# Kernel optimization log

Hardware: AMD Instinct MI355X
Metric: run time of the kernel (lower is better)

The kernel has to match this reference:

```python
import jax, jax.numpy as jnp
import numpy as np

H = 256      # hidden_dim
D = 64       # dim_dynamic
ND = 2       # num_dynamic
PR = 7       # pooler_resolution
S = PR * PR  # 49 spatial positions
B = 4800     # N * nr_boxes
P = H * D    # num_params
EPS = 1e-5


def setup_inputs() -> dict:
    key = jax.random.key(0)
    ks = jax.random.split(key, 32)
    def w(k, shape):
        return jax.random.normal(k, shape, dtype=jnp.float32) * 0.02
    inp = {
        "pro_features": jax.random.normal(ks[0], (1, B, H), jnp.float32),
        "roi_features": jax.random.normal(ks[1], (S, B, H), jnp.float32),
        "pos_xywh": jax.random.normal(ks[2], (1, B, H), jnp.float32),
        "pos_img": jax.random.normal(ks[3], (S, B, H), jnp.float32),
        "pos_local": jax.random.uniform(ks[4], (PR, PR), jnp.float32),
        "bboxes_xywh": jax.random.uniform(ks[5], (B, 4), jnp.float32, minval=0.2, maxval=1.0),
        # dynamic_layer: H -> ND*P
        "Wd": w(ks[6], (H, ND * P)), "bd": jnp.zeros((ND * P,), jnp.float32),
        # query_scale MLP (2 layers, H->H->H)
        "Wqs1": w(ks[7], (H, H)), "bqs1": jnp.zeros((H,), jnp.float32),
        "Wqs2": w(ks[8], (H, H)), "bqs2": jnp.zeros((H,), jnp.float32),
        # ref_point_head MLP (2 layers, H->H->2)
        "Wr1": w(ks[9], (H, H)), "br1": jnp.zeros((H,), jnp.float32),
        "Wr2": w(ks[10], (H, 2)), "br2": jnp.zeros((2,), jnp.float32),
        # ca_qpos_proj / ca_kpos_proj
        "Wq": w(ks[11], (H, H)), "bq": jnp.zeros((H,), jnp.float32),
        "Wk": w(ks[12], (H, H)), "bk": jnp.zeros((H,), jnp.float32),
        # layer norms
        "g1": jnp.ones((D,), jnp.float32), "be1": jnp.zeros((D,), jnp.float32),
        "g2": jnp.ones((H,), jnp.float32), "be2": jnp.zeros((H,), jnp.float32),
        "g3": jnp.ones((H,), jnp.float32), "be3": jnp.zeros((H,), jnp.float32),
        # out_layer: (H*S) -> H
        "Wo": w(ks[13], (H * S, H)), "bo": jnp.zeros((H,), jnp.float32),
    }
    return inp


def _ln(x, g, b):
    m = jnp.mean(x, axis=-1, keepdims=True)
    v = jnp.mean((x - m) ** 2, axis=-1, keepdims=True)
    return (x - m) * jax.lax.rsqrt(v + EPS) * g + b


def reference(pro_features, roi_features, pos_xywh, pos_img, pos_local, bboxes_xywh,
              Wd, bd, Wqs1, bqs1, Wqs2, bqs2, Wr1, br1, Wr2, br2,
              Wq, bq, Wk, bk, g1, be1, g2, be2, g3, be3, Wo, bo):
    # (S,B,H) -> (B,S,H)
    features_pos = jnp.transpose(pos_img @ Wq + bq, (1, 0, 2))
    features = jnp.transpose(roi_features, (1, 0, 2))
    # dynamic parameters: (1,B,ND*P) -> (B,1,ND*P)
    parameters = jnp.transpose(pro_features @ Wd + bd, (1, 0, 2))
    # query_scale MLP
    pos_t = jax.nn.relu(pro_features @ Wqs1 + bqs1) @ Wqs2 + bqs2  # (1,B,H)
    px = pos_xywh[..., :H] * pos_t                                 # (1,B,H)
    # ref_point_head -> sigmoid
    ref = jax.nn.sigmoid(jax.nn.relu(pro_features @ Wr1 + br1) @ Wr2 + br2)  # (1,B,2)
    bb = bboxes_xywh.reshape(1, -1, 4)
    hi = px[..., H // 2:] * (ref[..., 0] / bb[..., 2])[..., None]
    lo = px[..., :H // 2] * (ref[..., 1] / bb[..., 3])[..., None]
    px = jnp.concatenate([lo, hi], axis=-1)
    # (B,1,H) * (1,S,1) -> (B,S,H)
    px = jnp.transpose(px, (1, 0, 2)) * pos_local.reshape(-1)[None, :, None]
    param1_pos = px @ Wk + bk                                      # (B,S,H)
    param1 = parameters[:, :, :P].reshape(-1, H, D)                # (B,H,D)
    param2 = parameters[:, :, P:].reshape(-1, D, H)                # (B,D,H)
    f = jnp.einsum('bsh,bhd->bsd', features, param1)               # (B,S,D)
    fp = jnp.sum(features_pos * param1_pos, axis=-1)               # (B,S)
    f = f + fp[:, :, None]
    f = jax.nn.relu(_ln(f, g1, be1))
    f = jnp.einsum('bsd,bdh->bsh', f, param2)                      # (B,S,H)
    f = jax.nn.relu(_ln(f, g2, be2))
    f = f.reshape(f.shape[0], -1) @ Wo + bo                        # (B,H)
    f = jax.nn.relu(_ln(f, g3, be3))
    return f
```

## Files before the change

### kernel.cpp

```cpp
#include <hip/hip_runtime.h>
#include <hip/hip_bf16.h>

#define HH 256
#define DD 64
#define SS 49
#define BB 4800
#define PP 16384
#define NDP 32768
#define KWO 12544
#define MPAD 4864
#define SK 8
#define KCH 1568

typedef unsigned int u32;
typedef unsigned short u16;
typedef __attribute__((ext_vector_type(8))) short bf16x8;
typedef __attribute__((ext_vector_type(4))) float f32x4;

__device__ __forceinline__ float bf2f(__hip_bfloat16 h) { return __bfloat162float(h); }

__device__ __forceinline__ void load_lds16(const void* g, void* l) {
  __builtin_amdgcn_global_load_lds(
      (const __attribute__((address_space(1))) unsigned int*)g,
      (__attribute__((address_space(3))) unsigned int*)l, 16, 0, 0);
}

__device__ __forceinline__ int nperm(int n) {
  if (n < PP) { int h = n >> 6, d = n & 63; return d * HH + h; }
  int r = n - PP; int d = r >> 8, h = r & 255; return PP + h * DD + d;
}

__device__ __forceinline__ float wave_sum64(float v) {
#pragma unroll
  for (int off = 32; off > 0; off >>= 1) v += __shfl_xor(v, off);
  return v;
}

__device__ __forceinline__ float block_sum256(float v, float* red) {
  v = wave_sum64(v);
  int w = threadIdx.x >> 6;
  if ((threadIdx.x & 63) == 0) red[w] = v;
  __syncthreads();
  float r = red[0] + red[1] + red[2] + red[3];
  __syncthreads();
  return r;
}

__global__ void k0_prep(const float* __restrict__ Wq, const float* __restrict__ bk,
                        const float* __restrict__ bq, float* __restrict__ w2c2) {
  __shared__ float red[4];
  int k = blockIdx.x, h = threadIdx.x;
  float v = Wq[k * HH + h];
  float s = block_sum256(v * bk[h], red);
  if (h == 0) w2c2[k] = s;
  if (k == 0) {
    float s2 = block_sum256(bq[h] * bk[h], red);
    if (h == 0) w2c2[HH] = s2;
  }
}

__global__ __launch_bounds__(256) void kc_w1(
    const float* __restrict__ Wqs1, const float* __restrict__ Wqs2,
    const float* __restrict__ Wr1, const float* __restrict__ Wk,
    const float* __restrict__ Wq,
    u16* __restrict__ w1t, u16* __restrict__ w2t, u16* __restrict__ wr1t,
    u16* __restrict__ wkt, u16* __restrict__ wqh) {
  int t = threadIdx.x;
  int zi = blockIdx.z;
  if (zi == 4) {
    int row = blockIdx.y * 32 + (t >> 3), col = blockIdx.x * 32 + (t & 7) * 4;
    float4 v = *(const float4*)&Wq[row * HH + col];
    union { u16 u[4]; uint2 q; } pk;
    __hip_bfloat16 hb;
    hb = __float2bfloat16(v.x); pk.u[0] = *(u16*)&hb;
    hb = __float2bfloat16(v.y); pk.u[1] = *(u16*)&hb;
    hb = __float2bfloat16(v.z); pk.u[2] = *(u16*)&hb;
    hb = __float2bfloat16(v.w); pk.u[3] = *(u16*)&hb;
    *(uint2*)&wqh[row * HH + col] = pk.q;
    return;
  }
  const float* src = (zi == 0) ? Wqs1 : (zi == 1) ? Wqs2 : (zi == 2) ? Wr1 : Wk;
  u16* dst = (zi == 0) ? w1t : (zi == 1) ? w2t : (zi == 2) ? wr1t : wkt;
  __shared__ float tile[32][33];
  int n0 = blockIdx.x * 32, k0 = blockIdx.y * 32;
  {
    int kk = t >> 3, nn = (t & 7) * 4;
    float4 v = *(const float4*)&src[(k0 + kk) * HH + n0 + nn];
    tile[kk][nn + 0] = v.x;
    tile[kk][nn + 1] = v.y;
    tile[kk][nn + 2] = v.z;
    tile[kk][nn + 3] = v.w;
  }
  __syncthreads();
  {
    int nn = t >> 3, kk = (t & 7) * 4;
    union { u16 u[4]; uint2 q; } pk;
#pragma unroll
    for (int i = 0; i < 4; ++i) {
      __hip_bfloat16 hb = __float2bfloat16(tile[kk + i][nn]);
      pk.u[i] = *(u16*)&hb;
    }
    *(uint2*)&dst[(n0 + nn) * HH + k0 + kk] = pk.q;
  }
}

__device__ __forceinline__ void g_gemm(const u16* aLb, const u16* __restrict__ Bg,
                                       int wm, int wn, int lg, int lr,
                                       f32x4 acc[2][4]) {
#pragma unroll
  for (int k0 = 0; k0 < HH; k0 += 32) {
    int colb = (k0 + (lg << 3)) << 1;
    bf16x8 af[2];
#pragma unroll
    for (int mi = 0; mi < 2; ++mi) {
      int row = wm * 32 + mi * 16 + lr;
      af[mi] = *(const bf16x8*)((const char*)aLb + (row << 9) +
                                (colb ^ ((row & 7) << 4)));
    }
    bf16x8 bfr[4];
#pragma unroll
    for (int ni = 0; ni < 4; ++ni) {
      int n = wn * 64 + ni * 16 + lr;
      bfr[ni] = *(const bf16x8*)&Bg[n * HH + k0 + (lg << 3)];
    }
#pragma unroll
    for (int mi = 0; mi < 2; ++mi)
#pragma unroll
      for (int ni = 0; ni < 4; ++ni)
        acc[mi][ni] = __builtin_amdgcn_mfma_f32_16x16x32_bf16(af[mi], bfr[ni], acc[mi][ni], 0, 0, 0);
  }
}

__device__ __forceinline__ void c_write(u16* xLb, f32x4 acc[2][4],
                                        const float* __restrict__ bias, bool dorelu,
                                        int wm, int wn, int lg, int lr) {
#pragma unroll
  for (int ni = 0; ni < 4; ++ni) {
    int col = wn * 64 + ni * 16 + lr;
    float bv = bias ? bias[col] : 0.f;
#pragma unroll
    for (int mi = 0; mi < 2; ++mi) {
#pragma unroll
      for (int j = 0; j < 4; ++j) {
        int row = wm * 32 + mi * 16 + (lg << 2) + j;
        float v = acc[mi][ni][j] + bv;
        if (dorelu) v = fmaxf(v, 0.f);
        __hip_bfloat16 hb = __float2bfloat16(v);
        *(u16*)((char*)xLb + (row << 9) + (((col << 1)) ^ ((row & 7) << 4))) = *(u16*)&hb;
      }
    }
  }
}

__global__ __launch_bounds__(512) void k1_mfma(
    const u16* __restrict__ proh, const float* __restrict__ posx,
    const float* __restrict__ bbox,
    const u16* __restrict__ w1t, const u16* __restrict__ w2t,
    const u16* __restrict__ wr1t, const u16* __restrict__ wkt,
    const u16* __restrict__ wqh,
    const float* __restrict__ bqs1, const float* __restrict__ bqs2,
    const float* __restrict__ br1, const float* __restrict__ Wr2,
    const float* __restrict__ br2, const float* __restrict__ bq,
    float* __restrict__ z, float* __restrict__ c1) {
  __shared__ u16 aL[16384];
  __shared__ u16 xL[16384];
  __shared__ float red0[512], red1[512];
  __shared__ float scLoL[64], scHiL[64];
  const int t = threadIdx.x;
  const int w = t >> 6, l = t & 63;
  const int lg = l >> 4, lr = l & 15;
  const int wm = w >> 2, wn = w & 3;
  const int m0 = blockIdx.x * 64;

#pragma unroll
  for (int i = 0; i < 4; ++i) {
    int c = i * 512 + t;
    int a = c * 16;
    int row = a >> 9, x0 = a & 511;
    int src = (m0 + row) * HH + ((x0 ^ ((row & 7) << 4)) >> 1);
    load_lds16(proh + src, (char*)aL + (size_t)(i * 512 + (w << 6)) * 16);
  }
  __syncthreads();

  {
    f32x4 acc[2][4] = {};
    g_gemm(aL, wr1t, wm, wn, lg, lr, acc);
    c_write(xL, acc, br1, true, wm, wn, lg, lr);
  }
  __syncthreads();
  {
    int row = t & 63, seg = t >> 6;
    float s0 = 0.f, s1 = 0.f;
#pragma unroll 8
    for (int hh = 0; hh < 32; ++hh) {
      int h = seg * 32 + hh;
      float rv = bf2f(*(const __hip_bfloat16*)((const char*)xL + (row << 9) +
                                               (((h << 1)) ^ ((row & 7) << 4))));
      s0 = fmaf(rv, Wr2[h * 2 + 0], s0);
      s1 = fmaf(rv, Wr2[h * 2 + 1], s1);
    }
    red0[row * 8 + seg] = s0;
    red1[row * 8 + seg] = s1;
  }
  __syncthreads();
  if (t < 64) {
    float s0 = br2[0], s1 = br2[1];
#pragma unroll
    for (int k = 0; k < 8; ++k) {
      s0 += red0[t * 8 + k];
      s1 += red1[t * 8 + k];
    }
    float r0 = 1.f / (1.f + __expf(-s0));
    float r1 = 1.f / (1.f + __expf(-s1));
    scHiL[t] = r0 / bbox[(m0 + t) * 4 + 2];
    scLoL[t] = r1 / bbox[(m0 + t) * 4 + 3];
  }
  f32x4 acc1[2][4] = {};
  g_gemm(aL, w1t, wm, wn, lg, lr, acc1);
  __syncthreads();
  c_write(xL, acc1, bqs1, true, wm, wn, lg, lr);
  __syncthreads();
  f32x4 accp[2][4] = {};
  g_gemm(xL, w2t, wm, wn, lg, lr, accp);
  __syncthreads();
#pragma unroll
  for (int ni = 0; ni < 4; ++ni) {
    int col = wn * 64 + ni * 16 + lr;
    float bv = bqs2[col];
#pragma unroll
    for (int mi = 0; mi < 2; ++mi) {
#pragma unroll
      for (int j = 0; j < 4; ++j) {
        int row = wm * 32 + mi * 16 + (lg << 2) + j;
        float pt = accp[mi][ni][j] + bv;
        float sc = (col < 128) ? scLoL[row] : scHiL[row];
        float v = posx[(m0 + row) * HH + col] * pt * sc;
        __hip_bfloat16 hb = __float2bfloat16(v);
        *(u16*)((char*)aL + (row << 9) + (((col << 1)) ^ ((row & 7) << 4))) = *(u16*)&hb;
      }
    }
  }
  __syncthreads();
  {
    f32x4 acc[2][4] = {};
    g_gemm(aL, wkt, wm, wn, lg, lr, acc);
    c_write(xL, acc, nullptr, false, wm, wn, lg, lr);
  }
  __syncthreads();
  {
    int row = t & 63, seg = t >> 6;
    float s0 = 0.f;
#pragma unroll 8
    for (int hh = 0; hh < 32; ++hh) {
      int h = seg * 32 + hh;
      float yv = bf2f(*(const __hip_bfloat16*)((const char*)xL + (row << 9) +
                                               (((h << 1)) ^ ((row & 7) << 4))));
      s0 = fmaf(yv, bq[h], s0);
    }
    red0[row * 8 + seg] = s0;
  }
  f32x4 accz[2][4] = {};
  g_gemm(xL, wqh, wm, wn, lg, lr, accz);
  __syncthreads();
  if (t < 64) {
    float s = 0.f;
#pragma unroll
    for (int k = 0; k < 8; ++k) s += red0[t * 8 + k];
    c1[m0 + t] = s;
  }
#pragma unroll
  for (int ni = 0; ni < 4; ++ni) {
    int col = wn * 64 + ni * 16 + lr;
#pragma unroll
    for (int mi = 0; mi < 2; ++mi) {
#pragma unroll
      for (int j = 0; j < 4; ++j) {
        int row = wm * 32 + mi * 16 + (lg << 2) + j;
        z[(size_t)(m0 + row) * HH + col] = accz[mi][ni][j];
      }
    }
  }
}

__global__ __launch_bounds__(256) void k2_fp(
    const float* __restrict__ posi, const float* __restrict__ posl,
    const float* __restrict__ z, const float* __restrict__ c1,
    const float* __restrict__ w2c2, float* __restrict__ fp) {
  int b = blockIdx.x, t = threadIdx.x;
  int l = t & 63, w = t >> 6;
  float4 zv = *(const float4*)&z[b * HH + l * 4];
  float4 wv = *(const float4*)&w2c2[l * 4];
  float c1b = c1[b];
  float c2 = w2c2[HH];
  for (int s = w; s < SS; s += 4) {
    float4 pi = *(const float4*)&posi[((size_t)s * BB + b) * HH + l * 4];
    float d1 = pi.x * zv.x + pi.y * zv.y + pi.z * zv.z + pi.w * zv.w;
    float d2 = pi.x * wv.x + pi.y * wv.y + pi.z * wv.z + pi.w * wv.w;
#pragma unroll
    for (int off = 32; off > 0; off >>= 1) {
      d1 += __shfl_xor(d1, off);
      d2 += __shfl_xor(d2, off);
    }
    if (l == 0) fp[b * SS + s] = posl[s] * (d1 + c1b) + d2 + c2;
  }
}

__global__ __launch_bounds__(256) void kc_pro(const float* __restrict__ pro,
                                              u16* __restrict__ proh) {
  int tg = blockIdx.x * 256 + threadIdx.x;
  int e0 = tg * 8;
  int row = e0 >> 8;
  union { u16 u[8]; uint4 v; } pk;
  if (row < BB) {
    float4 v0 = *(const float4*)&pro[e0];
    float4 v1 = *(const float4*)&pro[e0 + 4];
    float vv[8] = {v0.x, v0.y, v0.z, v0.w, v1.x, v1.y, v1.z, v1.w};
#pragma unroll
    for (int i = 0; i < 8; ++i) {
      __hip_bfloat16 hb = __float2bfloat16(vv[i]);
      pk.u[i] = *(u16*)&hb;
    }
  } else {
    pk.v = make_uint4(0, 0, 0, 0);
  }
  *(uint4*)&proh[e0] = pk.v;
}

__global__ __launch_bounds__(256) void kc_wdt(const float* __restrict__ Wd,
                                              u16* __restrict__ wdt) {
  __shared__ float tile[32][33];
  int n0 = blockIdx.x * 32;
  int k0 = blockIdx.y * 32;
  int t = threadIdx.x;
  {
    int kk = t >> 3, nn = (t & 7) * 4;
    float4 v = *(const float4*)&Wd[(size_t)(k0 + kk) * NDP + n0 + nn];
    tile[kk][nn + 0] = v.x;
    tile[kk][nn + 1] = v.y;
    tile[kk][nn + 2] = v.z;
    tile[kk][nn + 3] = v.w;
  }
  __syncthreads();
  {
    int nn = t >> 3, kk = (t & 7) * 4;
    union { u16 u[4]; uint2 v; } pk;
#pragma unroll
    for (int i = 0; i < 4; ++i) {
      __hip_bfloat16 hb = __float2bfloat16(tile[kk + i][nn]);
      pk.u[i] = *(u16*)&hb;
    }
    int np = nperm(n0 + nn);
    *(uint2*)&wdt[(size_t)np * HH + k0 + kk] = pk.v;
  }
}

__global__ void kc_bdp(const float* __restrict__ bd, float* __restrict__ bdp) {
  int n = blockIdx.x * 256 + threadIdx.x;
  bdp[nperm(n)] = bd[n];
}

__global__ __launch_bounds__(256) void kc_wot(const float* __restrict__ Wo,
                                              u16* __restrict__ wot) {
  __shared__ float tile[32][33];
  int k0 = blockIdx.x * 32;
  int n0 = blockIdx.y * 32;
  int t = threadIdx.x;
  {
    int kk = t >> 3, nn = (t & 7) * 4;
    float4 v = *(const float4*)&Wo[(size_t)(k0 + kk) * HH + n0 + nn];
    tile[kk][nn + 0] = v.x;
    tile[kk][nn + 1] = v.y;
    tile[kk][nn + 2] = v.z;
    tile[kk][nn + 3] = v.w;
  }
  __syncthreads();
  {
    int nn = t >> 3, kk = (t & 7) * 4;
    union { u16 u[4]; uint2 v; } pk;
#pragma unroll
    for (int i = 0; i < 4; ++i) {
      __hip_bfloat16 hb = __float2bfloat16(tile[kk + i][nn]);
      pk.u[i] = *(u16*)&hb;
    }
    *(uint2*)&wot[(size_t)(n0 + nn) * KWO + k0 + kk] = pk.v;
  }
}

__global__ __launch_bounds__(256) void k3_mfma(const u16* __restrict__ proh,
                                               const u16* __restrict__ wdt,
                                               const float* __restrict__ bdp,
                                               u16* __restrict__ params) {
  __shared__ char smem[32768];
  u16* Al = (u16*)smem;
  u16* Bl = (u16*)(smem + 8192);
  const int t = threadIdx.x;
  const int w = t >> 6, l = t & 63;
  const int n0 = blockIdx.x * 128;
  const int m0 = blockIdx.y * 128;
  const int wr = w >> 1, wc = w & 1;
  f32x4 acc[4][4] = {};

  for (int k0 = 0; k0 < HH; k0 += 32) {
#pragma unroll
    for (int i = 0; i < 2; ++i) {
      int c = i * 256 + t;
      int r = c >> 2, kq = (c & 3) * 8;
      int wbase = (i * 256 + (w << 6)) * 8;
      load_lds16(proh + (size_t)(m0 + r) * HH + k0 + kq, Al + wbase);
      load_lds16(wdt + (size_t)(n0 + r) * HH + k0 + kq, Bl + wbase);
    }
    __syncthreads();
    bf16x8 af[4], bfr[4];
#pragma unroll
    for (int mi = 0; mi < 4; ++mi)
      af[mi] = *(const bf16x8*)&Al[(wr * 64 + mi * 16 + (l & 15)) * 32 + (l >> 4) * 8];
#pragma unroll
    for (int ni = 0; ni < 4; ++ni)
      bfr[ni] = *(const bf16x8*)&Bl[(wc * 64 + ni * 16 + (l & 15)) * 32 + (l >> 4) * 8];
#pragma unroll
    for (int mi = 0; mi < 4; ++mi)
#pragma unroll
      for (int ni = 0; ni < 4; ++ni)
        acc[mi][ni] = __builtin_amdgcn_mfma_f32_16x16x32_bf16(af[mi], bfr[ni], acc[mi][ni], 0, 0, 0);
    __syncthreads();
  }
  u16* cb = (u16*)smem;
#pragma unroll
  for (int ni = 0; ni < 4; ++ni) {
    int col = wc * 64 + ni * 16 + (l & 15);
    float bias = bdp[n0 + col];
#pragma unroll
    for (int mi = 0; mi < 4; ++mi) {
#pragma unroll
      for (int j = 0; j < 4; ++j) {
        int row = wr * 64 + mi * 16 + ((l >> 4) << 2) + j;
        __hip_bfloat16 hb = __float2bfloat16(acc[mi][ni][j] + bias);
        cb[row * 128 + col] = *(u16*)&hb;
      }
    }
  }
  __syncthreads();
#pragma unroll
  for (int i = 0; i < 8; ++i) {
    int idx = i * 256 + t;
    int row = idx >> 4, cc = (idx & 15) * 8;
    if (m0 + row < BB)
      *(uint4*)&params[(size_t)(m0 + row) * NDP + n0 + cc] = *(const uint4*)&cb[row * 128 + cc];
  }
}

__global__ __launch_bounds__(256) void k4_mfma(
    const float* __restrict__ roi, const u16* __restrict__ params,
    const float* __restrict__ fpbuf,
    const float* __restrict__ g1, const float* __restrict__ be1,
    const float* __restrict__ g2, const float* __restrict__ be2,
    u16* __restrict__ f2ws) {
  __shared__ u16 bufA[16384];
  __shared__ u16 bufP1[16384];
  __shared__ u16 f1L[4096];
  __shared__ float fpL[64];
  __shared__ float g1L[64], b1L[64], g2L[256], b2L[256];

  const int b = blockIdx.x;
  const int t = threadIdx.x;
  const int w = t >> 6, l = t & 63;
  const int lg = l >> 4, lr = l & 15;
  const int swz = (lr & 7) << 4;

#pragma unroll
  for (int i = 0; i < 8; ++i) {
    int c = i * 256 + t;
    int a = c * 16;
    int row = a >> 9;
    int x0 = a & 511;
    int src = b * NDP + row * HH + ((x0 ^ ((row & 7) << 4)) >> 1);
    load_lds16(params + src, (char*)bufP1 + (size_t)(i * 256 + (w << 6)) * 16);
  }
  uint4 p2r[8];
#pragma unroll
  for (int i = 0; i < 8; ++i) {
    int c = i * 256 + t;
    p2r[i] = *(const uint4*)&params[(size_t)b * NDP + PP + c * 8];
  }
#pragma unroll
  for (int i = 0; i < 16; ++i) {
    int idx = i * 256 + t;
    int row = idx >> 6, c4 = (idx & 63) << 2;
    union { u16 u[4]; unsigned long long v; } pk;
    if (row < SS) {
      float4 v = *(const float4*)&roi[((size_t)row * BB + b) * HH + c4];
      __hip_bfloat16 h0 = __float2bfloat16(v.x), h1 = __float2bfloat16(v.y);
      __hip_bfloat16 h2 = __float2bfloat16(v.z), h3 = __float2bfloat16(v.w);
      pk.u[0] = *(u16*)&h0; pk.u[1] = *(u16*)&h1;
      pk.u[2] = *(u16*)&h2; pk.u[3] = *(u16*)&h3;
    } else {
      pk.v = 0ull;
    }
    int ab = (row << 9) + (((c4 << 1)) ^ ((row & 7) << 4));
    *(unsigned long long*)((char*)bufA + ab) = pk.v;
  }
  if (t < 64) {
    fpL[t] = (t < SS) ? fpbuf[b * SS + t] : 0.f;
    g1L[t] = g1[t];
    b1L[t] = be1[t];
  }
  g2L[t] = g2[t];
  b2L[t] = be2[t];
  __syncthreads();

  f32x4 acc1[4] = {};
#pragma unroll
  for (int k0 = 0; k0 < HH; k0 += 32) {
    int colb = ((k0 + (lg << 3)) << 1) ^ swz;
    const bf16x8 af = *(const bf16x8*)((const char*)bufA + ((w * 16 + lr) << 9) + colb);
    bf16x8 bfr[4];
#pragma unroll
    for (int ni = 0; ni < 4; ++ni)
      bfr[ni] = *(const bf16x8*)((const char*)bufP1 + ((ni * 16 + lr) << 9) + colb);
#pragma unroll
    for (int ni = 0; ni < 4; ++ni)
      acc1[ni] = __builtin_amdgcn_mfma_f32_16x16x32_bf16(af, bfr[ni], acc1[ni], 0, 0, 0);
  }
  __syncthreads();

#pragma unroll
  for (int i = 0; i < 8; ++i) {
    int c = i * 256 + t;
    int a = c * 16;
    int row = a >> 7;
    int x0 = a & 127;
    *(uint4*)((char*)bufA + (row << 7) + (x0 ^ ((row & 7) << 4))) = p2r[i];
  }

#pragma unroll
  for (int j = 0; j < 4; ++j) {
    int s = w * 16 + (lg << 2) + j;
    float fpv = fpL[s];
    float x[4], sum = 0.f, sq = 0.f;
#pragma unroll
    for (int ni = 0; ni < 4; ++ni) {
      x[ni] = acc1[ni][j] + fpv;
      sum += x[ni];
      sq += x[ni] * x[ni];
    }
#pragma unroll
    for (int off = 1; off < 16; off <<= 1) {
      sum += __shfl_xor(sum, off);
      sq += __shfl_xor(sq, off);
    }
    float m = sum * (1.f / 64.f);
    float rs = rsqrtf(sq * (1.f / 64.f) - m * m + 1e-5f);
#pragma unroll
    for (int ni = 0; ni < 4; ++ni) {
      int d = ni * 16 + lr;
      float o = fmaxf((x[ni] - m) * rs * g1L[d] + b1L[d], 0.f);
      __hip_bfloat16 hb = __float2bfloat16(o);
      *(u16*)((char*)f1L + (s << 7) + ((d << 1) ^ ((s & 7) << 4))) = *(u16*)&hb;
    }
  }
  __syncthreads();

  f32x4 acc2[16] = {};
#pragma unroll
  for (int k0 = 0; k0 < 64; k0 += 32) {
    int colb = ((k0 + (lg << 3)) << 1) ^ swz;
    const bf16x8 af = *(const bf16x8*)((const char*)f1L + ((w * 16 + lr) << 7) + colb);
#pragma unroll
    for (int ni = 0; ni < 16; ++ni) {
      const bf16x8 bfr = *(const bf16x8*)((const char*)bufA + ((ni * 16 + lr) << 7) + colb);
      acc2[ni] = __builtin_amdgcn_mfma_f32_16x16x32_bf16(af, bfr, acc2[ni], 0, 0, 0);
    }
  }

#pragma unroll
  for (int j = 0; j < 4; ++j) {
    int s = w * 16 + (lg << 2) + j;
    float sum = 0.f, sq = 0.f;
#pragma unroll
    for (int ni = 0; ni < 16; ++ni) {
      float v = acc2[ni][j];
      sum += v;
      sq += v * v;
    }
#pragma unroll
    for (int off = 1; off < 16; off <<= 1) {
      sum += __shfl_xor(sum, off);
      sq += __shfl_xor(sq, off);
    }
    float m = sum * (1.f / 256.f);
    float rs = rsqrtf(sq * (1.f / 256.f) - m * m + 1e-5f);
    if (s < SS) {
#pragma unroll
      for (int ni = 0; ni < 16; ++ni) {
        int h = ni * 16 + lr;
        float o = fmaxf((acc2[ni][j] - m) * rs * g2L[h] + b2L[h], 0.f);
        __hip_bfloat16 hb = __float2bfloat16(o);
        f2ws[(size_t)b * KWO + s * HH + h] = *(u16*)&hb;
      }
    }
  }
}

__global__ __launch_bounds__(256) void k5_mfma(const u16* __restrict__ f2,
                                               const u16* __restrict__ wot,
                                               float* __restrict__ part) {
  __shared__ char smem[12288];
  u16* Al = (u16*)smem;
  u16* Bl = (u16*)(smem + 4096);
  const int t = threadIdx.x;
  const int w = t >> 6, l = t & 63;
  const int sk = blockIdx.x;
  const int m0 = blockIdx.y * 64;
  const int n0 = blockIdx.z * 128;
  const size_t kbase = (size_t)sk * KCH;
  const int wr = w >> 1, wc = w & 1;
  f32x4 acc[2][4] = {};

  for (int k0 = 0; k0 < KCH; k0 += 32) {
    {
      int r = t >> 2, kq = (t & 3) * 8;
      int wbase = (w << 6) * 8;
      load_lds16(f2 + (size_t)(m0 + r) * KWO + kbase + k0 + kq, Al + wbase);
    }
#pragma unroll
    for (int i = 0; i < 2; ++i) {
      int c = i * 256 + t;
      int r = c >> 2, kq = (c & 3) * 8;
      int wbase = (i * 256 + (w << 6)) * 8;
      load_lds16(wot + (size_t)(n0 + r) * KWO + kbase + k0 + kq, Bl + wbase);
    }
    __syncthreads();
    bf16x8 af[2], bfr[4];
#pragma unroll
    for (int mi = 0; mi < 2; ++mi)
      af[mi] = *(const bf16x8*)&Al[(wr * 32 + mi * 16 + (l & 15)) * 32 + (l >> 4) * 8];
#pragma unroll
    for (int ni = 0; ni < 4; ++ni)
      bfr[ni] = *(const bf16x8*)&Bl[(wc * 64 + ni * 16 + (l & 15)) * 32 + (l >> 4) * 8];
#pragma unroll
    for (int mi = 0; mi < 2; ++mi)
#pragma unroll
      for (int ni = 0; ni < 4; ++ni)
        acc[mi][ni] = __builtin_amdgcn_mfma_f32_16x16x32_bf16(af[mi], bfr[ni], acc[mi][ni], 0, 0, 0);
    __syncthreads();
  }
#pragma unroll
  for (int mi = 0; mi < 2; ++mi) {
#pragma unroll
    for (int j = 0; j < 4; ++j) {
      int m = m0 + wr * 32 + mi * 16 + ((l >> 4) << 2) + j;
#pragma unroll
      for (int ni = 0; ni < 4; ++ni) {
        int n = n0 + wc * 64 + ni * 16 + (l & 15);
        part[((size_t)sk * BB + m) * HH + n] = acc[mi][ni][j];
      }
    }
  }
}

__global__ __launch_bounds__(256) void k5r_ln3(
    const float* __restrict__ part, const float* __restrict__ bo,
    const float* __restrict__ g3, const float* __restrict__ be3,
    float* __restrict__ out) {
  __shared__ float red[4];
  int b = blockIdx.x, t = threadIdx.x;
  float v = bo[t];
#pragma unroll
  for (int sk = 0; sk < SK; ++sk) v += part[((size_t)sk * BB + b) * HH + t];
  float m = block_sum256(v, red) * (1.f / HH);
  float d = v - m;
  float var = block_sum256(d * d, red) * (1.f / HH);
  out[b * HH + t] = fmaxf(fmaf(d * rsqrtf(var + 1e-5f), g3[t], be3[t]), 0.f);
}

extern "C" void kernel_launch(void* const* d_in, const int* in_sizes, int n_in,
                              void* d_out, int out_size, void* d_ws, size_t ws_size,
                              hipStream_t stream) {
  const float* pro  = (const float*)d_in[0];
  const float* roi  = (const float*)d_in[1];
  const float* posx = (const float*)d_in[2];
  const float* posi = (const float*)d_in[3];
  const float* posl = (const float*)d_in[4];
  const float* bbox = (const float*)d_in[5];
  const float* Wd   = (const float*)d_in[6];
  const float* bd   = (const float*)d_in[7];
  const float* Wqs1 = (const float*)d_in[8];
  const float* bqs1 = (const float*)d_in[9];
  const float* Wqs2 = (const float*)d_in[10];
  const float* bqs2 = (const float*)d_in[11];
  const float* Wr1  = (const float*)d_in[12];
  const float* br1  = (const float*)d_in[13];
  const float* Wr2  = (const float*)d_in[14];
  const float* br2  = (const float*)d_in[15];
  const float* Wq   = (const float*)d_in[16];
  const float* bq   = (const float*)d_in[17];
  const float* Wk   = (const float*)d_in[18];
  const float* bk   = (const float*)d_in[19];
  const float* g1   = (const float*)d_in[20];
  const float* be1  = (const float*)d_in[21];
  const float* g2   = (const float*)d_in[22];
  const float* be2  = (const float*)d_in[23];
  const float* g3   = (const float*)d_in[24];
  const float* be3  = (const float*)d_in[25];
  const float* Wo   = (const float*)d_in[26];
  const float* bo   = (const float*)d_in[27];

  char* ws = (char*)d_ws;
  u16* w1t  = (u16*)(ws + 0ull);
  u16* w2t  = (u16*)(ws + 131072ull);
  u16* wr1t = (u16*)(ws + 262144ull);
  u16* wkt  = (u16*)(ws + 393216ull);
  u16* wqh  = (u16*)(ws + 524288ull);
  u16* params = (u16*)(ws + 0ull);
  float* part = (float*)(ws + 0ull);
  u16* f2ws   = (u16*)(ws + 314572800ull);
  u16* proh   = (u16*)(ws + 314572800ull);
  u16* wdt    = (u16*)(ws + 317063168ull);
  float* z    = (float*)(ws + 434995200ull);
  u16* wot    = (u16*)(ws + 434995200ull);
  float* bdp  = (float*)(ws + 441417728ull);
  float* fp   = (float*)(ws + 444825600ull);
  float* c1   = (float*)(ws + 445766400ull);
  float* w2c2 = (float*)(ws + 446047744ull);

  kc_pro<<<dim3(MPAD * HH / 8 / 256), dim3(256), 0, stream>>>(pro, proh);
  kc_w1<<<dim3(8, 8, 5), dim3(256), 0, stream>>>(Wqs1, Wqs2, Wr1, Wk, Wq,
                                                 w1t, w2t, wr1t, wkt, wqh);
  k0_prep<<<dim3(256), dim3(256), 0, stream>>>(Wq, bk, bq, w2c2);
  k1_mfma<<<dim3(BB / 64), dim3(512), 0, stream>>>(proh, posx, bbox, w1t, w2t, wr1t,
                                                   wkt, wqh, bqs1, bqs2, br1, Wr2,
                                                   br2, bq, z, c1);
  k2_fp<<<dim3(BB), dim3(256), 0, stream>>>(posi, posl, z, c1, w2c2, fp);
  kc_wot<<<dim3(KWO / 32, HH / 32), dim3(256), 0, stream>>>(Wo, wot);
  kc_wdt<<<dim3(NDP / 32, HH / 32), dim3(256), 0, stream>>>(Wd, wdt);
  kc_bdp<<<dim3(NDP / 256), dim3(256), 0, stream>>>(bd, bdp);
  k3_mfma<<<dim3(NDP / 128, MPAD / 128), dim3(256), 0, stream>>>(proh, wdt, bdp, params);
  k4_mfma<<<dim3(BB), dim3(256), 0, stream>>>(roi, params, fp, g1, be1, g2, be2, f2ws);
  k5_mfma<<<dim3(SK, BB / 64, HH / 128), dim3(256), 0, stream>>>(f2ws, wot, part);
  k5r_ln3<<<dim3(BB), dim3(256), 0, stream>>>(part, bo, g3, be3, (float*)d_out);
}
```

Before: 585.4 us.

## Shrink k4 LDS footprint by staging roi in halves and reusing buffers

Removes the separate bufA and f1L shared buffers in k4_mfma. The roi tile is now staged in two 128-column halves through a smaller bufF, which is later reused for the LayerNorm-1 output. param2 is loaded with async global-to-LDS copies into bufP1 once the first GEMM is done, so it no longer lives in 32 VGPRs. The goal is a smaller LDS and register footprint so more blocks fit per CU, at the cost of an extra barrier and less overlap of the roi and param2 loads with compute.

```diff
diff --git a/kernel.cpp b/kernel.cpp
--- a/kernel.cpp
+++ b/kernel.cpp
@@ -455,9 +455,8 @@
     const float* __restrict__ g1, const float* __restrict__ be1,
     const float* __restrict__ g2, const float* __restrict__ be2,
     u16* __restrict__ f2ws) {
-  __shared__ u16 bufA[16384];
   __shared__ u16 bufP1[16384];
-  __shared__ u16 f1L[4096];
+  __shared__ u16 bufF[8192];
   __shared__ float fpL[64];
   __shared__ float g1L[64], b1L[64], g2L[256], b2L[256];
 
@@ -465,27 +464,21 @@
   const int t = threadIdx.x;
   const int w = t >> 6, l = t & 63;
   const int lg = l >> 4, lr = l & 15;
-  const int swz = (lr & 7) << 4;
+  const u16* p1g = params + (size_t)b * NDP;
+  const u16* p2g = params + (size_t)b * NDP + PP;
 
 #pragma unroll
   for (int i = 0; i < 8; ++i) {
     int c = i * 256 + t;
     int a = c * 16;
-    int row = a >> 9;
-    int x0 = a & 511;
-    int src = b * NDP + row * HH + ((x0 ^ ((row & 7) << 4)) >> 1);
-    load_lds16(params + src, (char*)bufP1 + (size_t)(i * 256 + (w << 6)) * 16);
-  }
-  uint4 p2r[8];
+    int row = a >> 9, x0 = a & 511;
+    load_lds16(p1g + row * HH + ((x0 ^ ((row & 7) << 4)) >> 1),
+               (char*)bufP1 + (size_t)(i * 256 + (w << 6)) * 16);
+  }
 #pragma unroll
   for (int i = 0; i < 8; ++i) {
-    int c = i * 256 + t;
-    p2r[i] = *(const uint4*)&params[(size_t)b * NDP + PP + c * 8];
-  }
-#pragma unroll
-  for (int i = 0; i < 16; ++i) {
     int idx = i * 256 + t;
-    int row = idx >> 6, c4 = (idx & 63) << 2;
+    int row = idx >> 5, c4 = (idx & 31) << 2;
     union { u16 u[4]; unsigned long long v; } pk;
     if (row < SS) {
       float4 v = *(const float4*)&roi[((size_t)row * BB + b) * HH + c4];
@@ -496,8 +489,8 @@
     } else {
       pk.v = 0ull;
     }
-    int ab = (row << 9) + (((c4 << 1)) ^ ((row & 7) << 4));
-    *(unsigned long long*)((char*)bufA + ab) = pk.v;
+    int ab = (row << 8) + (((c4 << 1)) ^ ((row & 7) << 4));
+    *(unsigned long long*)((char*)bufF + ab) = pk.v;
   }
   if (t < 64) {
     fpL[t] = (t < SS) ? fpbuf[b * SS + t] : 0.f;
@@ -510,13 +503,52 @@
 
   f32x4 acc1[4] = {};
 #pragma unroll
-  for (int k0 = 0; k0 < HH; k0 += 32) {
-    int colb = ((k0 + (lg << 3)) << 1) ^ swz;
-    const bf16x8 af = *(const bf16x8*)((const char*)bufA + ((w * 16 + lr) << 9) + colb);
+  for (int k0 = 0; k0 < 128; k0 += 32) {
+    int arow = w * 16 + lr;
+    const bf16x8 af = *(const bf16x8*)((const char*)bufF + (arow << 8) +
+                                       ((((k0 + (lg << 3)) << 1)) ^ ((arow & 7) << 4)));
     bf16x8 bfr[4];
 #pragma unroll
+    for (int ni = 0; ni < 4; ++ni) {
+      int brow = ni * 16 + lr;
+      bfr[ni] = *(const bf16x8*)((const char*)bufP1 + (brow << 9) +
+                                 ((((k0 + (lg << 3)) << 1)) ^ ((brow & 7) << 4)));
+    }
+#pragma unroll
     for (int ni = 0; ni < 4; ++ni)
-      bfr[ni] = *(const bf16x8*)((const char*)bufP1 + ((ni * 16 + lr) << 9) + colb);
+      acc1[ni] = __builtin_amdgcn_mfma_f32_16x16x32_bf16(af, bfr[ni], acc1[ni], 0, 0, 0);
+  }
+  __syncthreads();
+#pragma unroll
+  for (int i = 0; i < 8; ++i) {
+    int idx = i * 256 + t;
+    int row = idx >> 5, c4 = (idx & 31) << 2;
+    union { u16 u[4]; unsigned long long v; } pk;
+    if (row < SS) {
+      float4 v = *(const float4*)&roi[((size_t)row * BB + b) * HH + 128 + c4];
+      __hip_bfloat16 h0 = __float2bfloat16(v.x), h1 = __float2bfloat16(v.y);
+      __hip_bfloat16 h2 = __float2bfloat16(v.z), h3 = __float2bfloat16(v.w);
+      pk.u[0] = *(u16*)&h0; pk.u[1] = *(u16*)&h1;
+      pk.u[2] = *(u16*)&h2; pk.u[3] = *(u16*)&h3;
+    } else {
+      pk.v = 0ull;
+    }
+    int ab = (row << 8) + (((c4 << 1)) ^ ((row & 7) << 4));
+    *(unsigned long long*)((char*)bufF + ab) = pk.v;
+  }
+  __syncthreads();
+#pragma unroll
+  for (int k0 = 0; k0 < 128; k0 += 32) {
+    int arow = w * 16 + lr;
+    const bf16x8 af = *(const bf16x8*)((const char*)bufF + (arow << 8) +
+                                       ((((k0 + (lg << 3)) << 1)) ^ ((arow & 7) << 4)));
+    bf16x8 bfr[4];
+#pragma unroll
+    for (int ni = 0; ni < 4; ++ni) {
+      int brow = ni * 16 + lr;
+      bfr[ni] = *(const bf16x8*)((const char*)bufP1 + (brow << 9) +
+                                 ((((128 + k0 + (lg << 3)) << 1)) ^ ((brow & 7) << 4)));
+    }
 #pragma unroll
     for (int ni = 0; ni < 4; ++ni)
       acc1[ni] = __builtin_amdgcn_mfma_f32_16x16x32_bf16(af, bfr[ni], acc1[ni], 0, 0, 0);
@@ -527,11 +559,12 @@
   for (int i = 0; i < 8; ++i) {
     int c = i * 256 + t;
     int a = c * 16;
-    int row = a >> 7;
-    int x0 = a & 127;
-    *(uint4*)((char*)bufA + (row << 7) + (x0 ^ ((row & 7) << 4))) = p2r[i];
-  }
-
+    int row = a >> 7, x0 = a & 127;
+    load_lds16(p2g + row * DD + ((x0 ^ ((row & 7) << 4)) >> 1),
+               (char*)bufP1 + (size_t)(i * 256 + (w << 6)) * 16);
+  }
+
+  u16* f1L = bufF;
 #pragma unroll
   for (int j = 0; j < 4; ++j) {
     int s = w * 16 + (lg << 2) + j;
@@ -563,11 +596,14 @@
   f32x4 acc2[16] = {};
 #pragma unroll
   for (int k0 = 0; k0 < 64; k0 += 32) {
-    int colb = ((k0 + (lg << 3)) << 1) ^ swz;
-    const bf16x8 af = *(const bf16x8*)((const char*)f1L + ((w * 16 + lr) << 7) + colb);
+    int arow = w * 16 + lr;
+    const bf16x8 af = *(const bf16x8*)((const char*)f1L + (arow << 7) +
+                                       ((((k0 + (lg << 3)) << 1)) ^ ((arow & 7) << 4)));
 #pragma unroll
     for (int ni = 0; ni < 16; ++ni) {
-      const bf16x8 bfr = *(const bf16x8*)((const char*)bufA + ((ni * 16 + lr) << 7) + colb);
+      int brow = ni * 16 + lr;
+      const bf16x8 bfr = *(const bf16x8*)((const char*)bufP1 + (brow << 7) +
+                                          ((((k0 + (lg << 3)) << 1)) ^ ((brow & 7) << 4)));
       acc2[ni] = __builtin_amdgcn_mfma_f32_16x16x32_bf16(af, bfr, acc2[ni], 0, 0, 0);
     }
   }
```

Result: faster. 534.3 us (-8.7%).
